# Optimization experiments

Hardware: AMD Instinct MI355X
Metric: run time of the kernel (lower is better)

## Reference

```python
import jax, jax.numpy as jnp
import numpy as np

D_MODEL = 1024
NUM_HEADS = 16
HEAD_DIM = D_MODEL // NUM_HEADS


def setup_inputs() -> dict:
    key = jax.random.key(0)
    ks = jax.random.split(key, 5)
    x = jax.random.normal(ks[0], (2, 2048, D_MODEL), dtype=jnp.float32)
    s = 1.0 / np.sqrt(D_MODEL)
    # nn.Linear weight is [out, in]; y = x @ W.T
    Wq = jax.random.normal(ks[1], (D_MODEL, D_MODEL), dtype=jnp.float32) * s
    Wk = jax.random.normal(ks[2], (D_MODEL, D_MODEL), dtype=jnp.float32) * s
    Wv = jax.random.normal(ks[3], (D_MODEL, D_MODEL), dtype=jnp.float32) * s
    Wo = jax.random.normal(ks[4], (D_MODEL, D_MODEL), dtype=jnp.float32) * s
    return {"x": x, "Wq": Wq, "Wk": Wk, "Wv": Wv, "Wo": Wo}


def reference(x, Wq, Wk, Wv, Wo):
    b, s, d = x.shape
    h, hd = NUM_HEADS, HEAD_DIM
    # projections (Linear: x @ W.T), reshape to [b, h, s, hd]
    def proj(W):
        return (x @ W.T).reshape(b, s, h, hd).transpose(0, 2, 1, 3)
    Q, K, V = proj(Wq), proj(Wk), proj(Wv)
    # NOTE: original scales by 1/sqrt(d_model), not 1/sqrt(head_dim)
    scores = jnp.einsum('bhqd,bhkd->bhqk', Q, K) / jnp.sqrt(jnp.float32(d))
    attn = jax.nn.softmax(scores, axis=-1)
    ctx = jnp.einsum('bhqk,bhkd->bhqd', attn, V)
    ctx = ctx.transpose(0, 2, 1, 3).reshape(b, s, d)
    return ctx @ Wo.T
```

## Files before the change

### kernel.cpp

```cpp
#include <hip/hip_runtime.h>
#include <cstddef>
#include <cstdint>

#define SEQ 2048
#define DM 1024
#define NH 16
#define HD 64

typedef _Float16 f16;
typedef __attribute__((ext_vector_type(8))) _Float16 f16x8;
typedef __attribute__((ext_vector_type(4))) _Float16 f16x4;
typedef __attribute__((ext_vector_type(2))) _Float16 f16x2;
typedef __attribute__((ext_vector_type(4))) float f32x4;

__global__ __launch_bounds__(256) void cast_all(const float* __restrict__ x,
                                                const float* __restrict__ Wq,
                                                const float* __restrict__ Wk,
                                                const float* __restrict__ Wv,
                                                const float* __restrict__ Wo,
                                                f16* __restrict__ dst) {
  const int i = blockIdx.x * 256 + threadIdx.x;
  const float* src;
  int off;
  if (i < 1048576) {
    src = x; off = i;
  } else {
    const int j = i - 1048576;
    const int wsel = j >> 18;
    src = (wsel == 0) ? Wq : (wsel == 1) ? Wk : (wsel == 2) ? Wv : Wo;
    off = j & 262143;
  }
  const float4 v = ((const float4*)src)[off];
  f16x4 o = {(f16)v.x, (f16)v.y, (f16)v.z, (f16)v.w};
  ((f16x4*)dst)[i] = o;
}

__device__ __forceinline__ void gload16(const void* g, void* lds) {
  __builtin_amdgcn_global_load_lds((const __attribute__((address_space(1))) void*)g,
                                   (__attribute__((address_space(3))) void*)lds,
                                   16, 0, 0);
}

__device__ __forceinline__ void gemm_tile_db(const f16* __restrict__ A,
                                             const f16* __restrict__ B,
                                             f16* As0, f16* Bs0,
                                             f16* As1, f16* Bs1,
                                             int K, f32x4 acc[4][4]) {
  const int t = threadIdx.x, lane = t & 63, w = t >> 6;
  const int wm = (w & 1) << 6, wn = (w >> 1) << 6;
  const int srow = lane >> 3, sg = lane & 7;
  const int fr = lane & 15, q = lane >> 4;
  const int scol = (sg ^ srow) << 3;
  auto stg = [&](int k0, f16* As, f16* Bs) {
#pragma unroll
    for (int c = 0; c < 4; ++c) {
      const int row = (w << 5) + (c << 3) + srow;
      gload16(A + (size_t)row * K + k0 + scol, As + (w << 11) + (c << 9));
      gload16(B + (size_t)row * K + k0 + scol, Bs + (w << 11) + (c << 9));
    }
  };
  auto comp = [&](const f16* As, const f16* Bs) {
    f16x8 af[4][2], bf[4][2];
#pragma unroll
    for (int i = 0; i < 4; ++i) {
      const int row = wm + (i << 4) + fr;
#pragma unroll
      for (int kh = 0; kh < 2; ++kh)
        af[i][kh] = *(const f16x8*)(As + row * 64 +
                                    ((((kh << 2) | q) ^ (row & 7)) << 3));
    }
#pragma unroll
    for (int j = 0; j < 4; ++j) {
      const int row = wn + (j << 4) + fr;
#pragma unroll
      for (int kh = 0; kh < 2; ++kh)
        bf[j][kh] = *(const f16x8*)(Bs + row * 64 +
                                    ((((kh << 2) | q) ^ (row & 7)) << 3));
    }
#pragma unroll
    for (int kh = 0; kh < 2; ++kh)
#pragma unroll
      for (int i = 0; i < 4; ++i)
#pragma unroll
        for (int j = 0; j < 4; ++j)
          acc[i][j] = __builtin_amdgcn_mfma_f32_16x16x32_f16(af[i][kh], bf[j][kh],
                                                             acc[i][j], 0, 0, 0);
  };
  stg(0, As0, Bs0);
  for (int k0 = 0; k0 < K; k0 += 128) {
    __syncthreads();
    stg(k0 + 64, As1, Bs1);
    comp(As0, Bs0);
    __syncthreads();
    if (k0 + 128 < K) stg(k0 + 128, As0, Bs0);
    comp(As1, Bs1);
  }
}

#define QSCALE 0.04508422003f
__global__ __launch_bounds__(256) void gemm_qkv(
    const f16* __restrict__ xb, const f16* __restrict__ Wqb,
    const f16* __restrict__ Wkb, const f16* __restrict__ Wvb,
    f16* __restrict__ Qb, f16* __restrict__ Kb, f16* __restrict__ Vtg) {
  __shared__ f16 smem[32768];
  f16* As0 = smem;
  f16* Bs0 = smem + 8192;
  f16* As1 = smem + 16384;
  f16* Bs1 = smem + 24576;
  const int which = blockIdx.x >> 3;
  const int bn = (blockIdx.x & 7) << 7;
  const int bm = blockIdx.y << 7;
  const f16* B = (which == 0) ? Wqb : (which == 1) ? Wkb : Wvb;
  f32x4 acc[4][4] = {};
  gemm_tile_db(xb + (size_t)bm * DM, B + (size_t)bn * DM, As0, Bs0, As1, Bs1,
               DM, acc);
  const int lane = threadIdx.x & 63, w = threadIdx.x >> 6;
  const int wm = (w & 1) << 6, wn = (w >> 1) << 6;
  const int col = lane & 15, q = lane >> 4;
  if (which < 2) {
    f16* C = (which == 0) ? Qb : Kb;
    const float sc = (which == 0) ? QSCALE : 1.0f;
#pragma unroll
    for (int i = 0; i < 4; ++i) {
      const int m = bm + wm + (i << 4) + (q << 2);
#pragma unroll
      for (int j = 0; j < 4; ++j) {
        const int n = bn + wn + (j << 4) + col;
#pragma unroll
        for (int r = 0; r < 4; ++r)
          C[(size_t)(m + r) * DM + n] = (f16)(acc[i][j][r] * sc);
      }
    }
  } else {
    __syncthreads();
#pragma unroll
    for (int i = 0; i < 4; ++i) {
      const int m0 = wm + (i << 4) + (q << 2);
      const int cm = m0 >> 3, sub = (m0 >> 2) & 1;
#pragma unroll
      for (int j = 0; j < 4; ++j) {
        const int nl = wn + (j << 4) + col;
        f16x4 o = {(f16)acc[i][j][0], (f16)acc[i][j][1],
                   (f16)acc[i][j][2], (f16)acc[i][j][3]};
        *(f16x4*)(smem + nl * 128 +
                  ((cm ^ (nl & 15) ^ ((nl >> 4) & 3)) << 3) + (sub << 2)) = o;
      }
    }
    __syncthreads();
    const int b = bm >> 11, sb = bm & 2047;
    const int d = threadIdx.x & 63;
#pragma unroll
    for (int pr = 0; pr < 8; ++pr) {
      const int idx0 = (threadIdx.x >> 6) + (pr << 3);
      const int hh = idx0 >> 5;
      const int s40 = idx0 & 31;
      const int s41 = s40 + 4;
      const int nl = (hh << 6) + d;
      f16x4 va, vb;
      {
        const int cm = s40 >> 1, sub = s40 & 1;
        va = *(const f16x4*)(smem + nl * 128 +
                             ((cm ^ (nl & 15) ^ ((nl >> 4) & 3)) << 3) + (sub << 2));
      }
      {
        const int cm = s41 >> 1, sub = s41 & 1;
        vb = *(const f16x4*)(smem + nl * 128 +
                             ((cm ^ (nl & 15) ^ ((nl >> 4) & 3)) << 3) + (sub << 2));
      }
      const int bh = (b << 4) + (bn >> 6) + hh;
      const int kt = (sb >> 6) + (s40 >> 4);
      const int kc2 = (s40 & 15) >> 3, qd = s40 & 3;
      const f16x8 vv = __builtin_shufflevector(va, vb, 0, 1, 2, 3, 4, 5, 6, 7);
      const size_t flat = ((size_t)bh << 17) + ((size_t)kt << 12) +
                          ((size_t)kc2 << 11) + ((size_t)qd << 9) + ((size_t)d << 3);
      *(f16x8*)(Vtg + flat) = vv;
    }
  }
}

__global__ __launch_bounds__(256) void gemm_out(const f16* __restrict__ Ab,
                                                const f16* __restrict__ Wob,
                                                float* __restrict__ out) {
  __shared__ f16 smem[24576];
  f16* As0 = smem;
  f16* As1 = smem + 8192;
  f16* Bs0 = smem + 16384;
  f16* Bs1 = smem + 20480;
  const int bn = blockIdx.x << 6, bm = blockIdx.y << 7;
  const int t = threadIdx.x, lane = t & 63, w = t >> 6;
  const int srow = lane >> 3, sg = lane & 7;
  const int fr = lane & 15, q = lane >> 4;
  const int scol = (sg ^ srow) << 3;
  const f16* A = Ab + (size_t)bm * DM;
  const f16* B = Wob + (size_t)bn * DM;
  const int wm = w << 5;
  f32x4 acc[2][4] = {};
  auto stg = [&](int k0, f16* As, f16* Bs) {
#pragma unroll
    for (int c = 0; c < 4; ++c) {
      const int row = (w << 5) + (c << 3) + srow;
      gload16(A + (size_t)row * DM + k0 + scol, As + (w << 11) + (c << 9));
    }
#pragma unroll
    for (int c = 0; c < 2; ++c) {
      const int row = (w << 4) + (c << 3) + srow;
      gload16(B + (size_t)row * DM + k0 + scol, Bs + (w << 10) + (c << 9));
    }
  };
  auto comp = [&](const f16* As, const f16* Bs) {
    f16x8 af[2][2], bf[4][2];
#pragma unroll
    for (int i = 0; i < 2; ++i) {
      const int row = wm + (i << 4) + fr;
#pragma unroll
      for (int kh = 0; kh < 2; ++kh)
        af[i][kh] = *(const f16x8*)(As + row * 64 +
                                    ((((kh << 2) | q) ^ (row & 7)) << 3));
    }
#pragma unroll
    for (int j = 0; j < 4; ++j) {
      const int row = (j << 4) + fr;
#pragma unroll
      for (int kh = 0; kh < 2; ++kh)
        bf[j][kh] = *(const f16x8*)(Bs + row * 64 +
                                    ((((kh << 2) | q) ^ (row & 7)) << 3));
    }
#pragma unroll
    for (int kh = 0; kh < 2; ++kh)
#pragma unroll
      for (int i = 0; i < 2; ++i)
#pragma unroll
        for (int j = 0; j < 4; ++j)
          acc[i][j] = __builtin_amdgcn_mfma_f32_16x16x32_f16(af[i][kh], bf[j][kh],
                                                             acc[i][j], 0, 0, 0);
  };
  stg(0, As0, Bs0);
  for (int k0 = 0; k0 < DM; k0 += 128) {
    __syncthreads();
    stg(k0 + 64, As1, Bs1);
    comp(As0, Bs0);
    __syncthreads();
    if (k0 + 128 < DM) stg(k0 + 128, As0, Bs0);
    comp(As1, Bs1);
  }
  const int col = lane & 15;
#pragma unroll
  for (int i = 0; i < 2; ++i) {
    const int m = bm + wm + (i << 4) + (q << 2);
#pragma unroll
    for (int j = 0; j < 4; ++j) {
      const int n = bn + (j << 4) + col;
#pragma unroll
      for (int r = 0; r < 4; ++r)
        out[(size_t)(m + r) * DM + n] = acc[i][j][r];
    }
  }
}

__global__ __launch_bounds__(256, 2) void attn_mfma(const f16* __restrict__ Qb,
                                                    const f16* __restrict__ Kb,
                                                    const f16* __restrict__ Vtg,
                                                    f16* __restrict__ Ctx) {
  __shared__ f16 smem[8192];
  const int t = threadIdx.x, lane = t & 63, w = t >> 6;
  const int fr = lane & 15, quad = lane >> 4;
  const int i = blockIdx.x;
  const int j = i >> 3;
  const int bh = ((i & 7) << 2) + (j >> 4);
  const int qt16 = j & 15;
  const int b = bh >> 4, h = bh & 15;

  const size_t qrow0 = (size_t)b * SEQ + qt16 * 128 + w * 32;

  f16x8 Qf[2][2];
#pragma unroll
  for (int qt = 0; qt < 2; ++qt)
#pragma unroll
    for (int hf = 0; hf < 2; ++hf)
      Qf[qt][hf] = *(const f16x8*)(Qb + (qrow0 + qt * 16 + fr) * DM + h * HD +
                                   hf * 32 + (quad << 3));

  const int krow = lane >> 2;
  const int kkc = ((lane & 3) - (lane >> 3)) & 3;
  const f16* Kg = Kb + ((size_t)b * SEQ + 16 * w + krow) * DM + h * HD + (kkc << 3);
  const f16* Vg = Vtg + ((size_t)bh << 17) + (quad << 9) + (fr << 3);

  const int crd = ((fr >> 1) << 3) | ((fr & 1) << 2) | (((fr >> 1) + quad) & 3);

  f16* K0 = smem;
  f16* K1 = smem + 4096;

  auto stageK = [&](int kt, f16* Kimg) {
#pragma unroll
    for (int hf = 0; hf < 2; ++hf)
      gload16(Kg + (size_t)kt * 64 * DM + hf * 32, Kimg + (hf << 11) + (w << 9));
  };

  f32x4 acc[2][4] = {};
  float lacc[2] = {0.f, 0.f};
  f16x8 Kf[4][2], pf[2][2];
  f16x8 va[4][2], vb[4][2];

  auto loadV = [&](int kt, f16x8 (&vr)[4][2]) {
#pragma unroll
    for (int dt = 0; dt < 4; ++dt)
#pragma unroll
      for (int kc = 0; kc < 2; ++kc)
        vr[dt][kc] = *(const f16x8*)(Vg + kt * 4096 + (kc << 11) + (dt << 7));
  };

  auto fragsK = [&](const f16* KR) {
#pragma unroll
    for (int mt = 0; mt < 4; ++mt)
#pragma unroll
      for (int hf = 0; hf < 2; ++hf)
        Kf[mt][hf] = *(const f16x8*)(KR + (crd << 3) + (hf << 11) + (mt << 9));
  };

  auto qkexp = [&]() {
    f32x4 z[2][4] = {};
#pragma unroll
    for (int hf = 0; hf < 2; ++hf)
#pragma unroll
      for (int qt = 0; qt < 2; ++qt)
#pragma unroll
        for (int mt = 0; mt < 4; ++mt)
          z[qt][mt] = __builtin_amdgcn_mfma_f32_16x16x32_f16(Kf[mt][hf], Qf[qt][hf],
                                                             z[qt][mt], 0, 0, 0);
#pragma unroll
    for (int qt = 0; qt < 2; ++qt) {
      f16x4 p4[4];
#pragma unroll
      for (int mt = 0; mt < 4; ++mt) {
        const float p0 = __builtin_amdgcn_exp2f(z[qt][mt][0]);
        const float p1 = __builtin_amdgcn_exp2f(z[qt][mt][1]);
        const float p2 = __builtin_amdgcn_exp2f(z[qt][mt][2]);
        const float p3 = __builtin_amdgcn_exp2f(z[qt][mt][3]);
        lacc[qt] += (p0 + p1) + (p2 + p3);
        const f16x2 lo = __builtin_bit_cast(f16x2, __builtin_amdgcn_cvt_pkrtz(p0, p1));
        const f16x2 hi = __builtin_bit_cast(f16x2, __builtin_amdgcn_cvt_pkrtz(p2, p3));
        f16x4 pv4; pv4.x = lo.x; pv4.y = lo.y; pv4.z = hi.x; pv4.w = hi.y;
        p4[mt] = pv4;
      }
      pf[qt][0] = __builtin_shufflevector(p4[0], p4[1], 0, 1, 2, 3, 4, 5, 6, 7);
      pf[qt][1] = __builtin_shufflevector(p4[2], p4[3], 0, 1, 2, 3, 4, 5, 6, 7);
    }
  };

  auto pv = [&](const f16x8 (&vr)[4][2]) {
#pragma unroll
    for (int kc = 0; kc < 2; ++kc)
#pragma unroll
      for (int dt = 0; dt < 4; ++dt)
#pragma unroll
        for (int qt = 0; qt < 2; ++qt)
          acc[qt][dt] = __builtin_amdgcn_mfma_f32_16x16x32_f16(vr[dt][kc], pf[qt][kc],
                                                               acc[qt][dt], 0, 0, 0);
  };

  stageK(0, K0);
  loadV(0, va);

  __syncthreads();
  stageK(1, K1);
  loadV(1, vb);
  fragsK(K0);
  qkexp();

  for (int kt = 1; kt < 31; kt += 2) {
    __syncthreads();
    stageK(kt + 1, K0);
    pv(va);
    loadV(kt + 1, va);
    fragsK(K1);
    qkexp();
    __syncthreads();
    if (kt + 2 < 32) stageK(kt + 2, K1);
    pv(vb);
    if (kt + 2 < 32) loadV(kt + 2, vb);
    fragsK(K0);
    qkexp();
  }

  __syncthreads();
  pv(va);
  fragsK(K1);
  qkexp();
  pv(vb);

  float inv[2];
#pragma unroll
  for (int qt = 0; qt < 2; ++qt) {
    float l = lacc[qt];
    l += __shfl_xor(l, 16);
    l += __shfl_xor(l, 32);
    inv[qt] = __builtin_amdgcn_rcpf(l);
  }

  __syncthreads();
  f16* T = smem + (w << 11);
#pragma unroll
  for (int qt = 0; qt < 2; ++qt)
#pragma unroll
    for (int dt = 0; dt < 4; ++dt) {
      f16x4 o = {(f16)(acc[qt][dt][0] * inv[qt]), (f16)(acc[qt][dt][1] * inv[qt]),
                 (f16)(acc[qt][dt][2] * inv[qt]), (f16)(acc[qt][dt][3] * inv[qt])};
      *(f16x4*)(T + (qt * 16 + fr) * 64 + dt * 16 + (quad << 2)) = o;
    }
#pragma unroll
  for (int p = 0; p < 4; ++p) {
    const int ql = p * 8 + (lane >> 3);
    const f16x8 v = *(const f16x8*)(T + ql * 64 + ((lane & 7) << 3));
    *(f16x8*)(Ctx + (qrow0 + ql) * DM + h * HD + ((lane & 7) << 3)) = v;
  }
}

extern "C" void kernel_launch(void* const* d_in, const int* in_sizes, int n_in,
                              void* d_out, int out_size, void* d_ws, size_t ws_size,
                              hipStream_t stream) {
  const float* x  = (const float*)d_in[0];
  const float* Wq = (const float*)d_in[1];
  const float* Wk = (const float*)d_in[2];
  const float* Wv = (const float*)d_in[3];
  const float* Wo = (const float*)d_in[4];

  char* ws = (char*)d_ws;
  f16* xb  = (f16*)(ws);
  f16* Wb  = (f16*)(ws + (8u << 20));
  f16* Wqb = Wb;
  f16* Wkb = Wb + 1048576;
  f16* Wvb = Wb + 2097152;
  f16* Wob = Wb + 3145728;
  f16* Qb  = (f16*)(ws + (16u << 20));
  f16* Kb  = (f16*)(ws + (24u << 20));
  f16* Vtg = (f16*)(ws + (32u << 20));
  f16* Ctx = (f16*)(ws + (40u << 20));

  cast_all<<<8192, 256, 0, stream>>>(x, Wq, Wk, Wv, Wo, xb);

  gemm_qkv<<<dim3(24, 32), 256, 0, stream>>>(xb, Wqb, Wkb, Wvb, Qb, Kb, Vtg);
  attn_mfma<<<dim3(2 * NH * (SEQ / 128)), 256, 0, stream>>>(Qb, Kb, Vtg, Ctx);
  gemm_out<<<dim3(16, 32), 256, 0, stream>>>(Ctx, Wob, (float*)d_out);
}
```

Measured before the change: 165.5 us.

## Pre-tile K into fragment layout and load attention K fragments directly from global

Adds a reshape_k kernel that rewrites K into a per-head, per-64-key-tile layout already arranged as MFMA fragments. The attention kernel then loads K fragments straight from global memory into registers instead of staging them through shared memory, which removes the block-wide barriers from the main loop. The loop is also restructured so the next tile's QK MFMAs are issued before the current tile's PV, with s_setprio raised around MFMA bursts. The cost is an extra kernel launch plus an extra pass over K in memory, and every wave now reads K from global/L2 on its own rather than sharing one staged copy.

```diff
diff --git a/kernel.cpp b/kernel.cpp
--- a/kernel.cpp
+++ b/kernel.cpp
@@ -178,6 +178,24 @@
   }
 }
 
+__global__ __launch_bounds__(256) void reshape_k(const f16* __restrict__ Kb,
+                                                 f16* __restrict__ Ktg) {
+  const int t = threadIdx.x, l = t & 63, w = t >> 6;
+  const int job = blockIdx.x * 4 + w;
+  const int bh = job >> 5, kt = job & 31;
+  const int b = bh >> 4, h = bh & 15;
+  const f16* src = Kb + (size_t)(b * SEQ + kt * 64 + (l & 15)) * DM + h * HD +
+                   ((l >> 4) << 3);
+  f16* dst = Ktg + ((size_t)bh << 17) + ((size_t)kt << 12) + (l << 3);
+#pragma unroll
+  for (int mt = 0; mt < 4; ++mt)
+#pragma unroll
+    for (int hf = 0; hf < 2; ++hf) {
+      const f16x8 v = *(const f16x8*)(src + (size_t)mt * 16 * DM + hf * 32);
+      *(f16x8*)(dst + mt * 1024 + hf * 512) = v;
+    }
+}
+
 __global__ __launch_bounds__(256) void gemm_out(const f16* __restrict__ Ab,
                                                 const f16* __restrict__ Wob,
                                                 float* __restrict__ out) {
@@ -258,7 +276,7 @@
 }
 
 __global__ __launch_bounds__(256, 2) void attn_mfma(const f16* __restrict__ Qb,
-                                                    const f16* __restrict__ Kb,
+                                                    const f16* __restrict__ Ktg,
                                                     const f16* __restrict__ Vtg,
                                                     f16* __restrict__ Ctx) {
   __shared__ f16 smem[8192];
@@ -280,45 +298,32 @@
       Qf[qt][hf] = *(const f16x8*)(Qb + (qrow0 + qt * 16 + fr) * DM + h * HD +
                                    hf * 32 + (quad << 3));
 
-  const int krow = lane >> 2;
-  const int kkc = ((lane & 3) - (lane >> 3)) & 3;
-  const f16* Kg = Kb + ((size_t)b * SEQ + 16 * w + krow) * DM + h * HD + (kkc << 3);
+  const f16* Kg = Ktg + ((size_t)bh << 17) + (lane << 3);
   const f16* Vg = Vtg + ((size_t)bh << 17) + (quad << 9) + (fr << 3);
-
-  const int crd = ((fr >> 1) << 3) | ((fr & 1) << 2) | (((fr >> 1) + quad) & 3);
-
-  f16* K0 = smem;
-  f16* K1 = smem + 4096;
-
-  auto stageK = [&](int kt, f16* Kimg) {
-#pragma unroll
-    for (int hf = 0; hf < 2; ++hf)
-      gload16(Kg + (size_t)kt * 64 * DM + hf * 32, Kimg + (hf << 11) + (w << 9));
-  };
 
   f32x4 acc[2][4] = {};
   float lacc[2] = {0.f, 0.f};
-  f16x8 Kf[4][2], pf[2][2];
-  f16x8 va[4][2], vb[4][2];
-
-  auto loadV = [&](int kt, f16x8 (&vr)[4][2]) {
+  f16x8 Kf[4][2];
+  f16x8 VfE[4][2], VfO[4][2];
+  f16x8 pfE[2][2], pfO[2][2];
+
+  auto loadK = [&](int kt) {
+#pragma unroll
+    for (int mt = 0; mt < 4; ++mt)
+#pragma unroll
+      for (int hf = 0; hf < 2; ++hf)
+        Kf[mt][hf] = *(const f16x8*)(Kg + kt * 4096 + mt * 1024 + hf * 512);
+  };
+  auto loadV = [&](int kt, f16x8 (&Vf)[4][2]) {
 #pragma unroll
     for (int dt = 0; dt < 4; ++dt)
 #pragma unroll
       for (int kc = 0; kc < 2; ++kc)
-        vr[dt][kc] = *(const f16x8*)(Vg + kt * 4096 + (kc << 11) + (dt << 7));
-  };
-
-  auto fragsK = [&](const f16* KR) {
-#pragma unroll
-    for (int mt = 0; mt < 4; ++mt)
-#pragma unroll
-      for (int hf = 0; hf < 2; ++hf)
-        Kf[mt][hf] = *(const f16x8*)(KR + (crd << 3) + (hf << 11) + (mt << 9));
-  };
-
-  auto qkexp = [&]() {
-    f32x4 z[2][4] = {};
+        Vf[dt][kc] = *(const f16x8*)(Vg + kt * 4096 + (kc << 11) + (dt << 7));
+  };
+
+  auto zmfma = [&](f32x4 (&z)[2][4]) {
+    __builtin_amdgcn_s_setprio(1);
 #pragma unroll
     for (int hf = 0; hf < 2; ++hf)
 #pragma unroll
@@ -327,6 +332,9 @@
         for (int mt = 0; mt < 4; ++mt)
           z[qt][mt] = __builtin_amdgcn_mfma_f32_16x16x32_f16(Kf[mt][hf], Qf[qt][hf],
                                                              z[qt][mt], 0, 0, 0);
+    __builtin_amdgcn_s_setprio(0);
+  };
+  auto expp = [&](f32x4 (&z)[2][4], f16x8 (&pf)[2][2]) {
 #pragma unroll
     for (int qt = 0; qt < 2; ++qt) {
       f16x4 p4[4];
@@ -346,47 +354,54 @@
       pf[qt][1] = __builtin_shufflevector(p4[2], p4[3], 0, 1, 2, 3, 4, 5, 6, 7);
     }
   };
-
-  auto pv = [&](const f16x8 (&vr)[4][2]) {
+  auto pv = [&](const f16x8 (&Vf)[4][2], const f16x8 (&pf)[2][2]) {
+    __builtin_amdgcn_s_setprio(1);
 #pragma unroll
     for (int kc = 0; kc < 2; ++kc)
 #pragma unroll
       for (int dt = 0; dt < 4; ++dt)
 #pragma unroll
         for (int qt = 0; qt < 2; ++qt)
-          acc[qt][dt] = __builtin_amdgcn_mfma_f32_16x16x32_f16(vr[dt][kc], pf[qt][kc],
+          acc[qt][dt] = __builtin_amdgcn_mfma_f32_16x16x32_f16(Vf[dt][kc], pf[qt][kc],
                                                                acc[qt][dt], 0, 0, 0);
-  };
-
-  stageK(0, K0);
-  loadV(0, va);
-
-  __syncthreads();
-  stageK(1, K1);
-  loadV(1, vb);
-  fragsK(K0);
-  qkexp();
-
+    __builtin_amdgcn_s_setprio(0);
+  };
+
+  loadK(0);
+  loadV(0, VfE);
+
+  {
+    f32x4 z[2][4] = {};
+    zmfma(z);
+    loadK(1);
+    loadV(1, VfO);
+    expp(z, pfE);
+  }
   for (int kt = 1; kt < 31; kt += 2) {
-    __syncthreads();
-    stageK(kt + 1, K0);
-    pv(va);
-    loadV(kt + 1, va);
-    fragsK(K1);
-    qkexp();
-    __syncthreads();
-    if (kt + 2 < 32) stageK(kt + 2, K1);
-    pv(vb);
-    if (kt + 2 < 32) loadV(kt + 2, vb);
-    fragsK(K0);
-    qkexp();
-  }
-
-  __syncthreads();
-  pv(va);
-  fragsK(K1);
-  qkexp();
-  pv(vb);
+    {
+      f32x4 z[2][4] = {};
+      zmfma(z);
+      loadK(kt + 1);
+      pv(VfE, pfE);
+      loadV(kt + 1, VfE);
+      expp(z, pfO);
+    }
+    {
+      f32x4 z[2][4] = {};
+      zmfma(z);
+      loadK(kt + 2);
+      pv(VfO, pfO);
+      loadV(kt + 2, VfO);
+      expp(z, pfE);
+    }
+  }
+  {
+    f32x4 z[2][4] = {};
+    zmfma(z);
+    pv(VfE, pfE);
+    expp(z, pfO);
+  }
+  pv(VfO, pfO);
 
   float inv[2];
 #pragma unroll
@@ -397,7 +412,6 @@
     inv[qt] = __builtin_amdgcn_rcpf(l);
   }
 
-  __syncthreads();
   f16* T = smem + (w << 11);
 #pragma unroll
   for (int qt = 0; qt < 2; ++qt)
@@ -407,6 +421,7 @@
                  (f16)(acc[qt][dt][2] * inv[qt]), (f16)(acc[qt][dt][3] * inv[qt])};
       *(f16x4*)(T + (qt * 16 + fr) * 64 + dt * 16 + (quad << 2)) = o;
     }
+  __builtin_amdgcn_s_waitcnt(0);
 #pragma unroll
   for (int p = 0; p < 4; ++p) {
     const int ql = p * 8 + (lane >> 3);
@@ -435,10 +450,12 @@
   f16* Kb  = (f16*)(ws + (24u << 20));
   f16* Vtg = (f16*)(ws + (32u << 20));
   f16* Ctx = (f16*)(ws + (40u << 20));
+  f16* Ktg = (f16*)(ws + (48u << 20));
 
   cast_all<<<8192, 256, 0, stream>>>(x, Wq, Wk, Wv, Wo, xb);
 
   gemm_qkv<<<dim3(24, 32), 256, 0, stream>>>(xb, Wqb, Wkb, Wvb, Qb, Kb, Vtg);
-  attn_mfma<<<dim3(2 * NH * (SEQ / 128)), 256, 0, stream>>>(Qb, Kb, Vtg, Ctx);
+  reshape_k<<<256, 256, 0, stream>>>(Kb, Ktg);
+  attn_mfma<<<dim3(2 * NH * (SEQ / 128)), 256, 0, stream>>>(Qb, Ktg, Vtg, Ctx);
   gemm_out<<<dim3(16, 32), 256, 0, stream>>>(Ctx, Wob, (float*)d_out);
 }
```

Measured after the change: 206.2 us. 1.25x slower.
